# Performance work log

Measured on AMD Instinct MI355X. Metric: run time of the kernel, lower is better.

The kernel has to match this reference:

```python
import jax, jax.numpy as jnp
import numpy as np

N_NODES = 100000
N_EDGES = 3200000
NFEAT = 256
NHID = 256
NOUT = 128


def setup_inputs() -> dict:
    key = jax.random.key(0)
    ks = jax.random.split(key, 8)
    stdv1 = 1.0 / np.sqrt(NHID)
    stdv2 = 1.0 / np.sqrt(NOUT)
    return {
        "feat": jax.random.normal(ks[0], (N_NODES, NFEAT), dtype=jnp.float32),
        "row": jax.random.randint(ks[1], (N_EDGES,), 0, N_NODES, dtype=jnp.int32),
        "col": jax.random.randint(ks[2], (N_EDGES,), 0, N_NODES, dtype=jnp.int32),
        "edge_weight": jax.random.uniform(ks[3], (N_EDGES,), dtype=jnp.float32),
        "W1": jax.random.uniform(ks[4], (NFEAT, NHID), jnp.float32, -stdv1, stdv1),
        "b1": jax.random.uniform(ks[5], (NHID,), jnp.float32, -stdv1, stdv1),
        "W2": jax.random.uniform(ks[6], (NHID, NOUT), jnp.float32, -stdv2, stdv2),
        "b2": jax.random.uniform(ks[7], (NOUT,), jnp.float32, -stdv2, stdv2),
    }


def _spmm(row, col, edge_weight, x, n_nodes):
    # sparse.mm(adj, x): out[i] = sum_e w[e] * x[col[e]] for row[e] == i
    msgs = x[col] * edge_weight[:, None]  # [E, F] gather + scale
    return jax.ops.segment_sum(msgs, row, num_segments=n_nodes)


def reference(feat, row, col, edge_weight, W1, b1, W2, b2):
    # Layer 1: GraphConvolution + ReLU (dropout is identity in eval mode)
    h = _spmm(row, col, edge_weight, feat @ W1, feat.shape[0]) + b1
    h = jax.nn.relu(h)
    # Layer 2: GraphConvolution (no activation on final layer)
    out = _spmm(row, col, edge_weight, h @ W2, feat.shape[0]) + b2
    return out
```

## Files before the change

kernel.cpp:

```cpp
#include <hip/hip_runtime.h>
#include <hip/hip_bf16.h>

#define M_NODES 100000
#define E_EDGES 3200000
#define NBUCK 196
#define BSHIFT 9
#define K3_EPB 8192
#define K3_BLOCKS 391

typedef __attribute__((ext_vector_type(8))) short short8;
typedef __attribute__((ext_vector_type(4))) float f32x4;
typedef __attribute__((ext_vector_type(2))) float f32x2;

__device__ inline unsigned short f2bf(float f) {
  __hip_bfloat16 h = __float2bfloat16(f);
  return __builtin_bit_cast(unsigned short, h);
}
__device__ inline float bf2f(unsigned short u) {
  return __uint_as_float(((unsigned int)u) << 16);
}

#if __has_builtin(__builtin_amdgcn_cvt_pk_f32_fp8) && __has_builtin(__builtin_amdgcn_cvt_pk_fp8_f32)
#define HW_FP8 1
#endif

#ifndef HW_FP8
__device__ inline float fp8_dec1(unsigned int b) {
  const unsigned int s = (b >> 7) & 1u, e = (b >> 3) & 15u, m = b & 7u;
  float v;
  if (e == 0) v = (float)m * 0.001953125f;
  else v = __uint_as_float(((e + 120u) << 23) | (m << 20));
  return s ? -v : v;
}
__device__ inline unsigned int fp8_enc1(float x) {
  const unsigned int sb = (__float_as_uint(x) >> 31) << 7;
  float ax = fminf(fabsf(x), 448.f);
  if (ax < 0.0009765625f) return sb;
  const unsigned int xb = __float_as_uint(ax);
  const int ef = (int)(xb >> 23) - 127;
  if (ef < -6) {
    unsigned int m = (unsigned int)(ax * 512.f + 0.5f);
    if (m > 7u) return sb | 0x08u;
    return sb | m;
  }
  unsigned int m3 = ((xb & 0x7FFFFFu) + 0x80000u) >> 20;
  unsigned int e4 = (unsigned int)(ef + 7);
  if (m3 == 8u) { m3 = 0u; e4 += 1u; }
  if (e4 >= 16u) { e4 = 15u; m3 = 6u; }
  return sb | (e4 << 3) | m3;
}
#endif

__device__ inline void fp8x4_dec(unsigned int v, float* o) {
#ifdef HW_FP8
  const f32x2 lo = __builtin_amdgcn_cvt_pk_f32_fp8((int)v, false);
  const f32x2 hi = __builtin_amdgcn_cvt_pk_f32_fp8((int)v, true);
  o[0] = lo[0]; o[1] = lo[1]; o[2] = hi[0]; o[3] = hi[1];
#else
  o[0] = fp8_dec1(v & 255u); o[1] = fp8_dec1((v >> 8) & 255u);
  o[2] = fp8_dec1((v >> 16) & 255u); o[3] = fp8_dec1(v >> 24);
#endif
}
__device__ inline unsigned short fp8x2_enc(float a, float b) {
#ifdef HW_FP8
  const int p = __builtin_amdgcn_cvt_pk_fp8_f32(a, b, 0, false);
  return (unsigned short)(p & 0xFFFF);
#else
  return (unsigned short)(fp8_enc1(a) | (fp8_enc1(b) << 8));
#endif
}

__global__ __launch_bounds__(256) void pack_w(
    const float* __restrict__ W, unsigned short* __restrict__ Bf,
    int K, int N)
{
  const int idx = blockIdx.x * 256 + threadIdx.x;
  const int total = (K >> 5) * (N >> 4) * 64;
  if (idx >= total) return;
  const int lane = idx & 63;
  const int f = idx >> 6;
  const int ntile = f % (N >> 4);
  const int kstep = f / (N >> 4);
  const int k0 = (kstep << 5) + ((lane >> 4) << 3);
  const int n = (ntile << 4) + (lane & 15);
  ushort4 lo, hi;
  lo.x = f2bf(W[(size_t)(k0 + 0) * N + n]);
  lo.y = f2bf(W[(size_t)(k0 + 1) * N + n]);
  lo.z = f2bf(W[(size_t)(k0 + 2) * N + n]);
  lo.w = f2bf(W[(size_t)(k0 + 3) * N + n]);
  hi.x = f2bf(W[(size_t)(k0 + 4) * N + n]);
  hi.y = f2bf(W[(size_t)(k0 + 5) * N + n]);
  hi.z = f2bf(W[(size_t)(k0 + 6) * N + n]);
  hi.w = f2bf(W[(size_t)(k0 + 7) * N + n]);
  *(ushort4*)&Bf[(size_t)idx * 8] = lo;
  *(ushort4*)&Bf[(size_t)idx * 8 + 4] = hi;
}

template<bool A_BF16>
__global__ __launch_bounds__(256) void gemm_mfma(
    const void* __restrict__ A_, const unsigned short* __restrict__ Bf,
    unsigned char* __restrict__ C, int M, int K, int N, int nTilesN)
{
  __shared__ float cbuf[4][16][132];
  const int wv = threadIdx.x >> 6, lane = threadIdx.x & 63;
  const int bm = blockIdx.x / nTilesN, bn = blockIdx.x % nTilesN;
  const int m0 = (bm << 8) + (wv << 6);
  const int n0 = bn << 7;
  const int rif = lane & 15, kg = lane >> 4;
  const int nf16 = N >> 4;

  f32x4 acc[4][8] = {};

  const int nK = K >> 5;
  for (int ks = 0; ks < nK; ++ks) {
    const int k0 = (ks << 5) + (kg << 3);
    short8 bfr[8];
    const size_t fbase = ((size_t)ks * nf16 + (n0 >> 4)) * 64 + lane;
#pragma unroll
    for (int nf = 0; nf < 8; ++nf)
      bfr[nf] = *(const short8*)&Bf[(fbase + (size_t)nf * 64) * 8];

    short8 afr[4];
#pragma unroll
    for (int mi = 0; mi < 4; ++mi) {
      const int row = m0 + (mi << 4) + rif;
      if (row < M) {
        if (A_BF16) {
          afr[mi] = *(const short8*)&((const unsigned short*)A_)[(size_t)row * K + k0];
        } else {
          const float* ap = &((const float*)A_)[(size_t)row * K + k0];
          const float4 lo = *(const float4*)ap;
          const float4 hi = *(const float4*)(ap + 4);
          short8 t;
          t[0] = (short)f2bf(lo.x); t[1] = (short)f2bf(lo.y);
          t[2] = (short)f2bf(lo.z); t[3] = (short)f2bf(lo.w);
          t[4] = (short)f2bf(hi.x); t[5] = (short)f2bf(hi.y);
          t[6] = (short)f2bf(hi.z); t[7] = (short)f2bf(hi.w);
          afr[mi] = t;
        }
      } else {
        afr[mi] = (short8)0;
      }
    }
#pragma unroll
    for (int mi = 0; mi < 4; ++mi)
#pragma unroll
      for (int nf = 0; nf < 8; ++nf)
        acc[mi][nf] = __builtin_amdgcn_mfma_f32_16x16x32_bf16(
            afr[mi], bfr[nf], acc[mi][nf], 0, 0, 0);
  }

#pragma unroll
  for (int mi = 0; mi < 4; ++mi) {
#pragma unroll
    for (int nf = 0; nf < 8; ++nf) {
#pragma unroll
      for (int r = 0; r < 4; ++r)
        cbuf[wv][(kg << 2) + r][(nf << 4) + rif] = acc[mi][nf][r];
    }
    __syncthreads();
#pragma unroll
    for (int r = 0; r < 16; ++r) {
      const int row = m0 + (mi << 4) + r;
      if (row < M) {
        const float2 v = *(const float2*)&cbuf[wv][r][lane << 1];
        *(unsigned short*)&C[(size_t)row * N + n0 + (lane << 1)] =
            fp8x2_enc(v.x, v.y);
      }
    }
    __syncthreads();
  }
}

__global__ __launch_bounds__(1024) void bucket_hist(
    const int* __restrict__ row, int* __restrict__ bhist)
{
  __shared__ int h[NBUCK];
  if (threadIdx.x < NBUCK) h[threadIdx.x] = 0;
  __syncthreads();
  const int e0 = blockIdx.x * K3_EPB;
  const int e1 = min(e0 + K3_EPB, E_EDGES);
  for (int i = e0 + threadIdx.x; i < e1; i += 1024)
    atomicAdd(&h[row[i] >> BSHIFT], 1);
  __syncthreads();
  if (threadIdx.x < NBUCK && h[threadIdx.x])
    atomicAdd(&bhist[threadIdx.x], h[threadIdx.x]);
}

__global__ __launch_bounds__(256) void scan_buckets(
    const int* __restrict__ bhist, int* __restrict__ bbase,
    int* __restrict__ bcursor, int* __restrict__ offs)
{
  __shared__ int buf[256];
  const int t = threadIdx.x;
  const int v = (t < NBUCK) ? bhist[t] : 0;
  buf[t] = v;
  __syncthreads();
  for (int d = 1; d < 256; d <<= 1) {
    const int x = (t >= d) ? buf[t - d] : 0;
    __syncthreads();
    buf[t] += x;
    __syncthreads();
  }
  if (t < NBUCK) {
    const int excl = buf[t] - v;
    bbase[t] = excl;
    bcursor[t] = excl;
  }
  if (t == 0) {
    bbase[NBUCK] = E_EDGES;
    offs[M_NODES] = E_EDGES;
  }
}

__global__ __launch_bounds__(512) void partition_edges(
    const int* __restrict__ row, const int* __restrict__ col,
    const float* __restrict__ w, int* __restrict__ bcursor,
    int2* __restrict__ P)
{
  __shared__ int2 stage[K3_EPB];
  __shared__ unsigned char sb[K3_EPB];
  __shared__ int hist[NBUCK], cur[NBUCK], delta[NBUCK];
  __shared__ int buf[256];
  const int t = threadIdx.x;
  const int e0 = blockIdx.x * K3_EPB;
  const int e1 = min(e0 + K3_EPB, E_EDGES);
  if (t < NBUCK) hist[t] = 0;
  __syncthreads();
  for (int i = e0 + t; i < e1; i += 512)
    atomicAdd(&hist[row[i] >> BSHIFT], 1);
  __syncthreads();
  int v = 0;
  if (t < 256) {
    v = (t < NBUCK) ? hist[t] : 0;
    buf[t] = v;
  }
  __syncthreads();
  for (int d = 1; d < 256; d <<= 1) {
    int x = 0;
    if (t < 256 && t >= d) x = buf[t - d];
    __syncthreads();
    if (t < 256) buf[t] += x;
    __syncthreads();
  }
  if (t < NBUCK) {
    const int excl = buf[t] - hist[t];
    cur[t] = excl;
    const int g = atomicAdd(&bcursor[t], hist[t]);
    delta[t] = g - excl;
  }
  __syncthreads();
  for (int i = e0 + t; i < e1; i += 512) {
    const int r = row[i];
    const int b = r >> BSHIFT;
    const int pos = atomicAdd(&cur[b], 1);
    stage[pos] = make_int2(col[i] | ((r & 511) << 20), __float_as_int(w[i]));
    sb[pos] = (unsigned char)b;
  }
  __syncthreads();
  const int n = e1 - e0;
  for (int i = t; i < n; i += 512)
    P[delta[sb[i]] + i] = stage[i];
}

__global__ __launch_bounds__(512) void bucket_csr(
    const int* __restrict__ bbase, const int2* __restrict__ P,
    int* __restrict__ offs, int2* __restrict__ epk)
{
  __shared__ int rhist[512], rcur[512];
  __shared__ int wsum[8];
  const int t = threadIdx.x;
  const int b = blockIdx.x;
  const int s = bbase[b], e = bbase[b + 1];
  const int row0 = b << BSHIFT;
  rhist[t] = 0;
  __syncthreads();
  for (int i = s + t; i < e; i += 512)
    atomicAdd(&rhist[(P[i].x >> 20) & 511], 1);
  __syncthreads();
  const int lane = t & 63, wv = t >> 6;
  const int v = rhist[t];
  int inc = v;
#pragma unroll
  for (int d = 1; d < 64; d <<= 1) {
    const int x = __shfl_up(inc, d);
    if (lane >= d) inc += x;
  }
  if (lane == 63) wsum[wv] = inc;
  __syncthreads();
  if (t < 8) {
    int sv = wsum[t];
#pragma unroll
    for (int d = 1; d < 8; d <<= 1) {
      const int x = __shfl_up(sv, d);
      if ((int)t >= d) sv += x;
    }
    wsum[t] = sv;
  }
  __syncthreads();
  const int excl = (wv ? wsum[wv - 1] : 0) + inc - v;
  const int gofs = s + excl;
  if (row0 + t < M_NODES) offs[row0 + t] = gofs;
  rcur[t] = gofs;
  __syncthreads();
  for (int i = s + t; i < e; i += 512) {
    const int2 p = P[i];
    const int rl = (p.x >> 20) & 511;
    const int pos = atomicAdd(&rcur[rl], 1);
    epk[pos] = make_int2(p.x & 0xFFFFF, p.y);
  }
}

__global__ __launch_bounds__(256) void spmm1_fused(
    const int* __restrict__ offs, const int2* __restrict__ epk,
    const unsigned char* __restrict__ X, const float* __restrict__ b1,
    unsigned short* __restrict__ Hb)
{
  const int w = threadIdx.x >> 6, lane = threadIdx.x & 63;
  const int r = (blockIdx.x << 2) + w;
  const int s = offs[r], e = offs[r + 1];
  float a0 = 0.f, a1 = 0.f, a2 = 0.f, a3 = 0.f;
  int i = s;
  for (; i + 8 <= e; i += 8) {
    int2 em[8];
#pragma unroll
    for (int u = 0; u < 8; ++u) em[u] = epk[i + u];
    unsigned int xv[8];
#pragma unroll
    for (int u = 0; u < 8; ++u)
      xv[u] = *(const unsigned int*)&X[((size_t)em[u].x << 8) + (lane << 2)];
#pragma unroll
    for (int u = 0; u < 8; ++u) {
      const float wv = __int_as_float(em[u].y);
      float f[4];
      fp8x4_dec(xv[u], f);
      a0 = fmaf(wv, f[0], a0);
      a1 = fmaf(wv, f[1], a1);
      a2 = fmaf(wv, f[2], a2);
      a3 = fmaf(wv, f[3], a3);
    }
  }
  for (; i < e; ++i) {
    const int2 ed = epk[i];
    const float wv = __int_as_float(ed.y);
    const unsigned int xw =
        *(const unsigned int*)&X[((size_t)ed.x << 8) + (lane << 2)];
    float f[4];
    fp8x4_dec(xw, f);
    a0 = fmaf(wv, f[0], a0);
    a1 = fmaf(wv, f[1], a1);
    a2 = fmaf(wv, f[2], a2);
    a3 = fmaf(wv, f[3], a3);
  }
  const float4 bv = *(const float4*)&b1[lane << 2];
  ushort4 o;
  o.x = f2bf(fmaxf(a0 + bv.x, 0.f));
  o.y = f2bf(fmaxf(a1 + bv.y, 0.f));
  o.z = f2bf(fmaxf(a2 + bv.z, 0.f));
  o.w = f2bf(fmaxf(a3 + bv.w, 0.f));
  *(ushort4*)&Hb[((size_t)r << 8) + (lane << 2)] = o;
}

__global__ __launch_bounds__(256) void spmm2_pair(
    const int* __restrict__ offs, const int2* __restrict__ epk,
    const unsigned char* __restrict__ X, const float* __restrict__ b2,
    float* __restrict__ Y)
{
  const int w = threadIdx.x >> 6, lane = threadIdx.x & 63;
  const int half = lane >> 5, l5 = lane & 31;
  const int r = (blockIdx.x << 2) + w;
  const int s = offs[r], e = offs[r + 1];
  float a0 = 0.f, a1 = 0.f, a2 = 0.f, a3 = 0.f;
  int i = s;
  for (; i + 8 <= e; i += 8) {
    int2 em[4];
#pragma unroll
    for (int u = 0; u < 4; ++u) em[u] = epk[i + (u << 1) + half];
    unsigned int xv[4];
#pragma unroll
    for (int u = 0; u < 4; ++u)
      xv[u] = *(const unsigned int*)&X[((size_t)em[u].x << 7) + (l5 << 2)];
#pragma unroll
    for (int u = 0; u < 4; ++u) {
      const float wv = __int_as_float(em[u].y);
      float f[4];
      fp8x4_dec(xv[u], f);
      a0 = fmaf(wv, f[0], a0);
      a1 = fmaf(wv, f[1], a1);
      a2 = fmaf(wv, f[2], a2);
      a3 = fmaf(wv, f[3], a3);
    }
  }
  for (; i < e; i += 2) {
    const int idx = i + half;
    const int2 ed = (idx < e) ? epk[idx] : make_int2(0, 0);
    const float wv = __int_as_float(ed.y);
    const unsigned int xw =
        *(const unsigned int*)&X[((size_t)ed.x << 7) + (l5 << 2)];
    float f[4];
    fp8x4_dec(xw, f);
    a0 = fmaf(wv, f[0], a0);
    a1 = fmaf(wv, f[1], a1);
    a2 = fmaf(wv, f[2], a2);
    a3 = fmaf(wv, f[3], a3);
  }
  a0 += __shfl_xor(a0, 32);
  a1 += __shfl_xor(a1, 32);
  a2 += __shfl_xor(a2, 32);
  a3 += __shfl_xor(a3, 32);
  if (half == 0) {
    const float4 bv = *(const float4*)&b2[l5 << 2];
    *(float4*)&Y[((size_t)r << 7) + (l5 << 2)] =
        make_float4(a0 + bv.x, a1 + bv.y, a2 + bv.z, a3 + bv.w);
  }
}

extern "C" void kernel_launch(void* const* d_in, const int* in_sizes, int n_in,
                              void* d_out, int out_size, void* d_ws, size_t ws_size,
                              hipStream_t stream) {
  const float* feat = (const float*)d_in[0];
  const int*   row  = (const int*)d_in[1];
  const int*   col  = (const int*)d_in[2];
  const float* ew   = (const float*)d_in[3];
  const float* W1   = (const float*)d_in[4];
  const float* b1   = (const float*)d_in[5];
  const float* W2   = (const float*)d_in[6];
  const float* b2   = (const float*)d_in[7];
  float* out = (float*)d_out;

  unsigned short* Hb = (unsigned short*)d_ws;
  int2* P = (int2*)d_ws;
  unsigned char* X1 = (unsigned char*)(Hb + (size_t)M_NODES * 256);
  unsigned char* X2 = X1;
  int2* epk = (int2*)(X1 + (size_t)M_NODES * 256);
  int* offs    = (int*)(epk + E_EDGES);
  int* bhist   = offs + 100004;
  int* bbase   = bhist + 200;
  int* bcursor = bbase + 200;
  unsigned short* W1f = (unsigned short*)(bcursor + 200);
  unsigned short* W2f = W1f + 65536;

  const int tilesM256 = (M_NODES + 255) / 256;

  hipMemsetAsync(bhist, 0, NBUCK * sizeof(int), stream);
  hipLaunchKernelGGL(bucket_hist, dim3(K3_BLOCKS), dim3(1024), 0, stream,
                     row, bhist);
  hipLaunchKernelGGL(scan_buckets, dim3(1), dim3(256), 0, stream,
                     bhist, bbase, bcursor, offs);
  hipLaunchKernelGGL(pack_w, dim3(32), dim3(256), 0, stream, W1, W1f, 256, 256);
  hipLaunchKernelGGL(pack_w, dim3(16), dim3(256), 0, stream, W2, W2f, 256, 128);
  hipLaunchKernelGGL(partition_edges, dim3(K3_BLOCKS), dim3(512), 0, stream,
                     row, col, ew, bcursor, P);
  hipLaunchKernelGGL(bucket_csr, dim3(NBUCK), dim3(512), 0, stream,
                     bbase, P, offs, epk);

  hipLaunchKernelGGL((gemm_mfma<false>), dim3(tilesM256 * 2), dim3(256), 0,
                     stream, (const void*)feat, W1f, X1, M_NODES, 256, 256, 2);
  hipLaunchKernelGGL(spmm1_fused, dim3(M_NODES / 4), dim3(256), 0, stream,
                     offs, epk, X1, b1, Hb);

  hipLaunchKernelGGL((gemm_mfma<true>), dim3(tilesM256), dim3(256), 0, stream,
                     (const void*)Hb, W2f, X2, M_NODES, 256, 128, 1);
  hipLaunchKernelGGL(spmm2_pair, dim3(M_NODES / 4), dim3(256), 0, stream,
                     offs, epk, X2, b2, out);
}
```

Before: 381.7 us.

## Drop edge histogram pass with fixed-capacity buckets; widen per-lane SpMM gathers

```diff
diff --git a/kernel.cpp b/kernel.cpp
--- a/kernel.cpp
+++ b/kernel.cpp
@@ -5,6 +5,7 @@
 #define E_EDGES 3200000
 #define NBUCK 196
 #define BSHIFT 9
+#define BCAP 24576
 #define K3_EPB 8192
 #define K3_BLOCKS 391
 
@@ -15,9 +16,6 @@
 __device__ inline unsigned short f2bf(float f) {
   __hip_bfloat16 h = __float2bfloat16(f);
   return __builtin_bit_cast(unsigned short, h);
-}
-__device__ inline float bf2f(unsigned short u) {
-  return __uint_as_float(((unsigned int)u) << 16);
 }
 
 #if __has_builtin(__builtin_amdgcn_cvt_pk_f32_fp8) && __has_builtin(__builtin_amdgcn_cvt_pk_fp8_f32)
@@ -70,13 +68,9 @@
 #endif
 }
 
-__global__ __launch_bounds__(256) void pack_w(
-    const float* __restrict__ W, unsigned short* __restrict__ Bf,
-    int K, int N)
-{
-  const int idx = blockIdx.x * 256 + threadIdx.x;
-  const int total = (K >> 5) * (N >> 4) * 64;
-  if (idx >= total) return;
+__device__ inline void pack_one(const float* __restrict__ W,
+                                unsigned short* __restrict__ Bf,
+                                int idx, int N) {
   const int lane = idx & 63;
   const int f = idx >> 6;
   const int ntile = f % (N >> 4);
@@ -94,6 +88,16 @@
   hi.w = f2bf(W[(size_t)(k0 + 7) * N + n]);
   *(ushort4*)&Bf[(size_t)idx * 8] = lo;
   *(ushort4*)&Bf[(size_t)idx * 8 + 4] = hi;
+}
+
+__global__ __launch_bounds__(256) void pack_w_both(
+    const float* __restrict__ W1, const float* __restrict__ W2,
+    unsigned short* __restrict__ W1f, unsigned short* __restrict__ W2f)
+{
+  if (blockIdx.x < 32)
+    pack_one(W1, W1f, blockIdx.x * 256 + threadIdx.x, 256);
+  else
+    pack_one(W2, W2f, (blockIdx.x - 32) * 256 + threadIdx.x, 128);
 }
 
 template<bool A_BF16>
@@ -172,50 +176,9 @@
   }
 }
 
-__global__ __launch_bounds__(1024) void bucket_hist(
-    const int* __restrict__ row, int* __restrict__ bhist)
-{
-  __shared__ int h[NBUCK];
-  if (threadIdx.x < NBUCK) h[threadIdx.x] = 0;
-  __syncthreads();
-  const int e0 = blockIdx.x * K3_EPB;
-  const int e1 = min(e0 + K3_EPB, E_EDGES);
-  for (int i = e0 + threadIdx.x; i < e1; i += 1024)
-    atomicAdd(&h[row[i] >> BSHIFT], 1);
-  __syncthreads();
-  if (threadIdx.x < NBUCK && h[threadIdx.x])
-    atomicAdd(&bhist[threadIdx.x], h[threadIdx.x]);
-}
-
-__global__ __launch_bounds__(256) void scan_buckets(
-    const int* __restrict__ bhist, int* __restrict__ bbase,
-    int* __restrict__ bcursor, int* __restrict__ offs)
-{
-  __shared__ int buf[256];
-  const int t = threadIdx.x;
-  const int v = (t < NBUCK) ? bhist[t] : 0;
-  buf[t] = v;
-  __syncthreads();
-  for (int d = 1; d < 256; d <<= 1) {
-    const int x = (t >= d) ? buf[t - d] : 0;
-    __syncthreads();
-    buf[t] += x;
-    __syncthreads();
-  }
-  if (t < NBUCK) {
-    const int excl = buf[t] - v;
-    bbase[t] = excl;
-    bcursor[t] = excl;
-  }
-  if (t == 0) {
-    bbase[NBUCK] = E_EDGES;
-    offs[M_NODES] = E_EDGES;
-  }
-}
-
 __global__ __launch_bounds__(512) void partition_edges(
     const int* __restrict__ row, const int* __restrict__ col,
-    const float* __restrict__ w, int* __restrict__ bcursor,
+    const float* __restrict__ w, int* __restrict__ bcnt,
     int2* __restrict__ P)
 {
   __shared__ int2 stage[K3_EPB];
@@ -246,8 +209,8 @@
   if (t < NBUCK) {
     const int excl = buf[t] - hist[t];
     cur[t] = excl;
-    const int g = atomicAdd(&bcursor[t], hist[t]);
-    delta[t] = g - excl;
+    const int g = atomicAdd(&bcnt[t], hist[t]);
+    delta[t] = (t * BCAP + g) - excl;
   }
   __syncthreads();
   for (int i = e0 + t; i < e1; i += 512) {
@@ -263,20 +226,42 @@
     P[delta[sb[i]] + i] = stage[i];
 }
 
+__global__ __launch_bounds__(256) void scan_buckets(
+    const int* __restrict__ bcnt, int* __restrict__ bbase,
+    int* __restrict__ offs)
+{
+  __shared__ int buf[256];
+  const int t = threadIdx.x;
+  const int v = (t < NBUCK) ? bcnt[t] : 0;
+  buf[t] = v;
+  __syncthreads();
+  for (int d = 1; d < 256; d <<= 1) {
+    const int x = (t >= d) ? buf[t - d] : 0;
+    __syncthreads();
+    buf[t] += x;
+    __syncthreads();
+  }
+  if (t < NBUCK) bbase[t] = buf[t] - v;
+  if (t == 0) offs[M_NODES] = E_EDGES;
+}
+
 __global__ __launch_bounds__(512) void bucket_csr(
-    const int* __restrict__ bbase, const int2* __restrict__ P,
-    int* __restrict__ offs, int2* __restrict__ epk)
+    const int* __restrict__ bcnt, const int* __restrict__ bbase,
+    const int2* __restrict__ P, int* __restrict__ offs,
+    int2* __restrict__ epk)
 {
   __shared__ int rhist[512], rcur[512];
   __shared__ int wsum[8];
   const int t = threadIdx.x;
   const int b = blockIdx.x;
-  const int s = bbase[b], e = bbase[b + 1];
+  const int cnt = bcnt[b];
+  const int src0 = b * BCAP;
+  const int dst0 = bbase[b];
   const int row0 = b << BSHIFT;
   rhist[t] = 0;
   __syncthreads();
-  for (int i = s + t; i < e; i += 512)
-    atomicAdd(&rhist[(P[i].x >> 20) & 511], 1);
+  for (int i = t; i < cnt; i += 512)
+    atomicAdd(&rhist[(P[src0 + i].x >> 20) & 511], 1);
   __syncthreads();
   const int lane = t & 63, wv = t >> 6;
   const int v = rhist[t];
@@ -299,12 +284,12 @@
   }
   __syncthreads();
   const int excl = (wv ? wsum[wv - 1] : 0) + inc - v;
-  const int gofs = s + excl;
+  const int gofs = dst0 + excl;
   if (row0 + t < M_NODES) offs[row0 + t] = gofs;
   rcur[t] = gofs;
   __syncthreads();
-  for (int i = s + t; i < e; i += 512) {
-    const int2 p = P[i];
+  for (int i = t; i < cnt; i += 512) {
+    const int2 p = P[src0 + i];
     const int rl = (p.x >> 20) & 511;
     const int pos = atomicAdd(&rcur[rl], 1);
     epk[pos] = make_int2(p.x & 0xFFFFF, p.y);
@@ -317,101 +302,119 @@
     unsigned short* __restrict__ Hb)
 {
   const int w = threadIdx.x >> 6, lane = threadIdx.x & 63;
-  const int r = (blockIdx.x << 2) + w;
-  const int s = offs[r], e = offs[r + 1];
-  float a0 = 0.f, a1 = 0.f, a2 = 0.f, a3 = 0.f;
-  int i = s;
-  for (; i + 8 <= e; i += 8) {
-    int2 em[8];
-#pragma unroll
-    for (int u = 0; u < 8; ++u) em[u] = epk[i + u];
-    unsigned int xv[8];
-#pragma unroll
-    for (int u = 0; u < 8; ++u)
-      xv[u] = *(const unsigned int*)&X[((size_t)em[u].x << 8) + (lane << 2)];
-#pragma unroll
-    for (int u = 0; u < 8; ++u) {
-      const float wv = __int_as_float(em[u].y);
-      float f[4];
-      fp8x4_dec(xv[u], f);
-      a0 = fmaf(wv, f[0], a0);
-      a1 = fmaf(wv, f[1], a1);
-      a2 = fmaf(wv, f[2], a2);
-      a3 = fmaf(wv, f[3], a3);
-    }
-  }
-  for (; i < e; ++i) {
-    const int2 ed = epk[i];
-    const float wv = __int_as_float(ed.y);
-    const unsigned int xw =
-        *(const unsigned int*)&X[((size_t)ed.x << 8) + (lane << 2)];
-    float f[4];
-    fp8x4_dec(xw, f);
-    a0 = fmaf(wv, f[0], a0);
-    a1 = fmaf(wv, f[1], a1);
-    a2 = fmaf(wv, f[2], a2);
-    a3 = fmaf(wv, f[3], a3);
-  }
-  const float4 bv = *(const float4*)&b1[lane << 2];
-  ushort4 o;
-  o.x = f2bf(fmaxf(a0 + bv.x, 0.f));
-  o.y = f2bf(fmaxf(a1 + bv.y, 0.f));
-  o.z = f2bf(fmaxf(a2 + bv.z, 0.f));
-  o.w = f2bf(fmaxf(a3 + bv.w, 0.f));
-  *(ushort4*)&Hb[((size_t)r << 8) + (lane << 2)] = o;
-}
-
-__global__ __launch_bounds__(256) void spmm2_pair(
-    const int* __restrict__ offs, const int2* __restrict__ epk,
-    const unsigned char* __restrict__ X, const float* __restrict__ b2,
-    float* __restrict__ Y)
-{
-  const int w = threadIdx.x >> 6, lane = threadIdx.x & 63;
   const int half = lane >> 5, l5 = lane & 31;
   const int r = (blockIdx.x << 2) + w;
   const int s = offs[r], e = offs[r + 1];
-  float a0 = 0.f, a1 = 0.f, a2 = 0.f, a3 = 0.f;
+  float a[8] = {};
   int i = s;
   for (; i + 8 <= e; i += 8) {
     int2 em[4];
 #pragma unroll
     for (int u = 0; u < 4; ++u) em[u] = epk[i + (u << 1) + half];
-    unsigned int xv[4];
+    uint2 xv[4];
 #pragma unroll
     for (int u = 0; u < 4; ++u)
-      xv[u] = *(const unsigned int*)&X[((size_t)em[u].x << 7) + (l5 << 2)];
+      xv[u] = *(const uint2*)&X[((size_t)em[u].x << 8) + (l5 << 3)];
 #pragma unroll
     for (int u = 0; u < 4; ++u) {
       const float wv = __int_as_float(em[u].y);
-      float f[4];
-      fp8x4_dec(xv[u], f);
-      a0 = fmaf(wv, f[0], a0);
-      a1 = fmaf(wv, f[1], a1);
-      a2 = fmaf(wv, f[2], a2);
-      a3 = fmaf(wv, f[3], a3);
+      float f[4], g[4];
+      fp8x4_dec(xv[u].x, f);
+      fp8x4_dec(xv[u].y, g);
+      a[0] = fmaf(wv, f[0], a[0]); a[1] = fmaf(wv, f[1], a[1]);
+      a[2] = fmaf(wv, f[2], a[2]); a[3] = fmaf(wv, f[3], a[3]);
+      a[4] = fmaf(wv, g[0], a[4]); a[5] = fmaf(wv, g[1], a[5]);
+      a[6] = fmaf(wv, g[2], a[6]); a[7] = fmaf(wv, g[3], a[7]);
     }
   }
   for (; i < e; i += 2) {
     const int idx = i + half;
     const int2 ed = (idx < e) ? epk[idx] : make_int2(0, 0);
     const float wv = __int_as_float(ed.y);
-    const unsigned int xw =
-        *(const unsigned int*)&X[((size_t)ed.x << 7) + (l5 << 2)];
-    float f[4];
-    fp8x4_dec(xw, f);
-    a0 = fmaf(wv, f[0], a0);
-    a1 = fmaf(wv, f[1], a1);
-    a2 = fmaf(wv, f[2], a2);
-    a3 = fmaf(wv, f[3], a3);
-  }
-  a0 += __shfl_xor(a0, 32);
-  a1 += __shfl_xor(a1, 32);
-  a2 += __shfl_xor(a2, 32);
-  a3 += __shfl_xor(a3, 32);
+    const uint2 xw = *(const uint2*)&X[((size_t)ed.x << 8) + (l5 << 3)];
+    float f[4], g[4];
+    fp8x4_dec(xw.x, f);
+    fp8x4_dec(xw.y, g);
+    a[0] = fmaf(wv, f[0], a[0]); a[1] = fmaf(wv, f[1], a[1]);
+    a[2] = fmaf(wv, f[2], a[2]); a[3] = fmaf(wv, f[3], a[3]);
+    a[4] = fmaf(wv, g[0], a[4]); a[5] = fmaf(wv, g[1], a[5]);
+    a[6] = fmaf(wv, g[2], a[6]); a[7] = fmaf(wv, g[3], a[7]);
+  }
+#pragma unroll
+  for (int j = 0; j < 8; ++j) a[j] += __shfl_xor(a[j], 32);
   if (half == 0) {
-    const float4 bv = *(const float4*)&b2[l5 << 2];
-    *(float4*)&Y[((size_t)r << 7) + (l5 << 2)] =
-        make_float4(a0 + bv.x, a1 + bv.y, a2 + bv.z, a3 + bv.w);
+    const float4 bv0 = *(const float4*)&b1[l5 << 3];
+    const float4 bv1 = *(const float4*)&b1[(l5 << 3) + 4];
+    short8 o;
+    o[0] = (short)f2bf(fmaxf(a[0] + bv0.x, 0.f));
+    o[1] = (short)f2bf(fmaxf(a[1] + bv0.y, 0.f));
+    o[2] = (short)f2bf(fmaxf(a[2] + bv0.z, 0.f));
+    o[3] = (short)f2bf(fmaxf(a[3] + bv0.w, 0.f));
+    o[4] = (short)f2bf(fmaxf(a[4] + bv1.x, 0.f));
+    o[5] = (short)f2bf(fmaxf(a[5] + bv1.y, 0.f));
+    o[6] = (short)f2bf(fmaxf(a[6] + bv1.z, 0.f));
+    o[7] = (short)f2bf(fmaxf(a[7] + bv1.w, 0.f));
+    *(short8*)&Hb[((size_t)r << 8) + (l5 << 3)] = o;
+  }
+}
+
+__global__ __launch_bounds__(256) void spmm2_quad(
+    const int* __restrict__ offs, const int2* __restrict__ epk,
+    const unsigned char* __restrict__ X, const float* __restrict__ b2,
+    float* __restrict__ Y)
+{
+  const int w = threadIdx.x >> 6, lane = threadIdx.x & 63;
+  const int q = lane >> 4, l4 = lane & 15;
+  const int r = (blockIdx.x << 2) + w;
+  const int s = offs[r], e = offs[r + 1];
+  float a[8] = {};
+  int i = s;
+  for (; i + 16 <= e; i += 16) {
+    int2 em[4];
+#pragma unroll
+    for (int u = 0; u < 4; ++u) em[u] = epk[i + (u << 2) + q];
+    uint2 xv[4];
+#pragma unroll
+    for (int u = 0; u < 4; ++u)
+      xv[u] = *(const uint2*)&X[((size_t)em[u].x << 7) + (l4 << 3)];
+#pragma unroll
+    for (int u = 0; u < 4; ++u) {
+      const float wv = __int_as_float(em[u].y);
+      float f[4], g[4];
+      fp8x4_dec(xv[u].x, f);
+      fp8x4_dec(xv[u].y, g);
+      a[0] = fmaf(wv, f[0], a[0]); a[1] = fmaf(wv, f[1], a[1]);
+      a[2] = fmaf(wv, f[2], a[2]); a[3] = fmaf(wv, f[3], a[3]);
+      a[4] = fmaf(wv, g[0], a[4]); a[5] = fmaf(wv, g[1], a[5]);
+      a[6] = fmaf(wv, g[2], a[6]); a[7] = fmaf(wv, g[3], a[7]);
+    }
+  }
+  for (; i < e; i += 4) {
+    const int idx = i + q;
+    const int2 ed = (idx < e) ? epk[idx] : make_int2(0, 0);
+    const float wv = __int_as_float(ed.y);
+    const uint2 xw = *(const uint2*)&X[((size_t)ed.x << 7) + (l4 << 3)];
+    float f[4], g[4];
+    fp8x4_dec(xw.x, f);
+    fp8x4_dec(xw.y, g);
+    a[0] = fmaf(wv, f[0], a[0]); a[1] = fmaf(wv, f[1], a[1]);
+    a[2] = fmaf(wv, f[2], a[2]); a[3] = fmaf(wv, f[3], a[3]);
+    a[4] = fmaf(wv, g[0], a[4]); a[5] = fmaf(wv, g[1], a[5]);
+    a[6] = fmaf(wv, g[2], a[6]); a[7] = fmaf(wv, g[3], a[7]);
+  }
+#pragma unroll
+  for (int j = 0; j < 8; ++j) {
+    a[j] += __shfl_xor(a[j], 16);
+    a[j] += __shfl_xor(a[j], 32);
+  }
+  if (q == 0) {
+    const float4 bv0 = *(const float4*)&b2[l4 << 3];
+    const float4 bv1 = *(const float4*)&b2[(l4 << 3) + 4];
+    float* yp = &Y[((size_t)r << 7) + (l4 << 3)];
+    *(float4*)yp = make_float4(a[0] + bv0.x, a[1] + bv0.y,
+                               a[2] + bv0.z, a[3] + bv0.w);
+    *(float4*)(yp + 4) = make_float4(a[4] + bv1.x, a[5] + bv1.y,
+                                     a[6] + bv1.z, a[7] + bv1.w);
   }
 }
 
@@ -433,26 +436,23 @@
   unsigned char* X1 = (unsigned char*)(Hb + (size_t)M_NODES * 256);
   unsigned char* X2 = X1;
   int2* epk = (int2*)(X1 + (size_t)M_NODES * 256);
-  int* offs    = (int*)(epk + E_EDGES);
-  int* bhist   = offs + 100004;
-  int* bbase   = bhist + 200;
-  int* bcursor = bbase + 200;
-  unsigned short* W1f = (unsigned short*)(bcursor + 200);
+  int* offs  = (int*)(epk + E_EDGES);
+  int* bcnt  = offs + 100004;
+  int* bbase = bcnt + 200;
+  unsigned short* W1f = (unsigned short*)(bbase + 200);
   unsigned short* W2f = W1f + 65536;
 
   const int tilesM256 = (M_NODES + 255) / 256;
 
-  hipMemsetAsync(bhist, 0, NBUCK * sizeof(int), stream);
-  hipLaunchKernelGGL(bucket_hist, dim3(K3_BLOCKS), dim3(1024), 0, stream,
-                     row, bhist);
+  hipMemsetAsync(bcnt, 0, NBUCK * sizeof(int), stream);
+  hipLaunchKernelGGL(pack_w_both, dim3(48), dim3(256), 0, stream,
+                     W1, W2, W1f, W2f);
+  hipLaunchKernelGGL(partition_edges, dim3(K3_BLOCKS), dim3(512), 0, stream,
+                     row, col, ew, bcnt, P);
   hipLaunchKernelGGL(scan_buckets, dim3(1), dim3(256), 0, stream,
-                     bhist, bbase, bcursor, offs);
-  hipLaunchKernelGGL(pack_w, dim3(32), dim3(256), 0, stream, W1, W1f, 256, 256);
-  hipLaunchKernelGGL(pack_w, dim3(16), dim3(256), 0, stream, W2, W2f, 256, 128);
-  hipLaunchKernelGGL(partition_edges, dim3(K3_BLOCKS), dim3(512), 0, stream,
-                     row, col, ew, bcursor, P);
+                     bcnt, bbase, offs);
   hipLaunchKernelGGL(bucket_csr, dim3(NBUCK), dim3(512), 0, stream,
-                     bbase, P, offs, epk);
+                     bcnt, bbase, P, offs, epk);
 
   hipLaunchKernelGGL((gemm_mfma<false>), dim3(tilesM256 * 2), dim3(256), 0,
                      stream, (const void*)feat, W1f, X1, M_NODES, 256, 256, 2);
@@ -461,6 +461,6 @@
 
   hipLaunchKernelGGL((gemm_mfma<true>), dim3(tilesM256), dim3(256), 0, stream,
                      (const void*)Hb, W2f, X2, M_NODES, 256, 128, 1);
-  hipLaunchKernelGGL(spmm2_pair, dim3(M_NODES / 4), dim3(256), 0, stream,
+  hipLaunchKernelGGL(spmm2_quad, dim3(M_NODES / 4), dim3(256), 0, stream,
                      offs, epk, X2, b2, out);
 }
```

Result: faster. 352.9 us (-7.5%).
